# Optimization experiments

Hardware: AMD Instinct MI355X
Metric: run time of the kernel (lower is better)

Reference implementation:

```python
import jax, jax.numpy as jnp
import numpy as np

B, S, E, H = 4, 2048, 1024, 16
D = E // H  # head dim = 64


def setup_inputs() -> dict:
    key = jax.random.key(0)
    ks = jax.random.split(key, 9)
    sc = 1.0 / np.sqrt(E)
    x = jax.random.normal(ks[0], (B, S, E), dtype=jnp.float32)
    # causal mask: 1 = keep, 0 = masked -> -inf (matches masked_fill(mask==0, -inf))
    mask = jnp.broadcast_to(jnp.tril(jnp.ones((S, S), dtype=jnp.int32)), (B, S, S))
    return {
        "x": x,
        "mask": mask,
        "wq": jax.random.normal(ks[1], (E, E), dtype=jnp.float32) * sc,
        "bq": jax.random.normal(ks[2], (E,), dtype=jnp.float32) * sc,
        "wk": jax.random.normal(ks[3], (E, E), dtype=jnp.float32) * sc,
        "bk": jax.random.normal(ks[4], (E,), dtype=jnp.float32) * sc,
        "wv": jax.random.normal(ks[5], (E, E), dtype=jnp.float32) * sc,
        "bv": jax.random.normal(ks[6], (E,), dtype=jnp.float32) * sc,
        "wo": jax.random.normal(ks[7], (E, E), dtype=jnp.float32) * sc,
        "bo": jax.random.normal(ks[8], (E,), dtype=jnp.float32) * sc,
    }


def reference(x, mask, wq, bq, wk, bk, wv, bv, wo, bo):
    # nn.Linear: y = x @ W^T + b
    def proj(w, b):
        y = jnp.einsum('bse,fe->bsf', x, w) + b
        return y.reshape(B, S, H, D).transpose(0, 2, 1, 3)  # [B,H,S,D]

    q = proj(wq, bq)
    k = proj(wk, bk)
    v = proj(wv, bv)
    denom = jnp.asarray(np.sqrt(D), dtype=x.dtype)
    score = jnp.einsum('bhqd,bhkd->bhqk', q, k) / denom  # [B,H,S,S]
    score = jnp.where(mask[:, None, :, :] == 0, jnp.asarray(-jnp.inf, score.dtype), score)
    attn = jax.nn.softmax(score, axis=-1)
    out = jnp.einsum('bhqk,bhkd->bhqd', attn, v)  # [B,H,S,D]
    out = out.transpose(0, 2, 1, 3).reshape(B, S, E)
    return jnp.einsum('bse,fe->bsf', out, wo) + bo
```

## Files before the change

kernel.cpp:

```cpp
#include <hip/hip_runtime.h>
#include <cstdint>
#include <cstddef>

typedef unsigned short u16;
typedef __bf16 bf16;
typedef bf16 bf16x8 __attribute__((ext_vector_type(8)));
typedef bf16 bf16x4 __attribute__((ext_vector_type(4)));
typedef float f32x4 __attribute__((ext_vector_type(4)));
typedef u16 u16x8 __attribute__((ext_vector_type(8)));
typedef u16 u16x4 __attribute__((ext_vector_type(4)));

#define ASYNC16(g, l) __builtin_amdgcn_global_load_lds( \
    (const __attribute__((address_space(1))) void*)(g), \
    (__attribute__((address_space(3))) void*)(l), 16, 0, 0)

#define FENCE asm volatile("" ::: "memory")
#define BARRIER do { FENCE; __builtin_amdgcn_s_barrier(); FENCE; } while (0)
#define WAITVM(n) asm volatile("s_waitcnt vmcnt(" #n ")" ::: "memory")

__device__ __forceinline__ u16 f2bf(float f) {
  bf16 h = (bf16)f;
  return __builtin_bit_cast(u16, h);
}

__device__ __forceinline__ u16x4 pk4(float a, float b, float c, float d) {
  bf16x4 v = { (bf16)a, (bf16)b, (bf16)c, (bf16)d };
  return __builtin_bit_cast(u16x4, v);
}

__device__ __forceinline__ void store_out(u16* p, float v) { *p = f2bf(v); }
__device__ __forceinline__ void store_out(float* p, float v) { *p = v; }

__device__ __forceinline__ f32x4 mfma16(bf16x8 a, bf16x8 b, f32x4 c) {
  return __builtin_amdgcn_mfma_f32_16x16x32_bf16(a, b, c, 0, 0, 0);
}

__global__ void prep(const float* __restrict__ x,  const float* __restrict__ wq,
                     const float* __restrict__ wk, const float* __restrict__ wv,
                     const float* __restrict__ wo, const float* __restrict__ bq,
                     const float* __restrict__ bk,
                     u16* __restrict__ xb, u16* __restrict__ wqkb,
                     u16* __restrict__ wvb, u16* __restrict__ wob,
                     float* __restrict__ bqk, float scl)
{
  const int bid = blockIdx.x, tid = threadIdx.x;
  if (bid < 8192) {
    int i = bid * 256 + tid;
    float4 v = ((const float4*)x)[i];
    ((u16x4*)xb)[i] = pk4(v.x, v.y, v.z, v.w);
  } else if (bid < 12288) {
    int wsel = (bid - 8192) >> 10;
    int i = ((bid - 8192) & 1023) * 256 + tid;
    const float* src = wsel == 0 ? wq : wsel == 1 ? wk : wsel == 2 ? wv : wo;
    u16* dst = wsel == 0 ? wqkb : wsel == 1 ? wqkb + 1048576 : wsel == 2 ? wvb : wob;
    float s = wsel == 0 ? scl : 1.0f;
    float4 v = ((const float4*)src)[i];
    ((u16x4*)dst)[i] = pk4(v.x * s, v.y * s, v.z * s, v.w * s);
  } else {
    for (int i = tid; i < 1024; i += 256) {
      bqk[i] = bq[i] * scl;
      bqk[1024 + i] = bk[i];
    }
  }
}

template <typename OutT>
__device__ __forceinline__ void gemm256(
    u16* sA, u16* sB,
    const u16* __restrict__ A, const u16* __restrict__ Bm,
    const float* __restrict__ bias_col, const float* __restrict__ bias_row,
    OutT* __restrict__ C, int M, int N, int K, int bm, int bn)
{
  const int tid = threadIdx.x;
  const int w = tid >> 6, lane = tid & 63;
  const int quad = lane >> 4, l15 = lane & 15;
  const int wr = w >> 2, wc = w & 3;

  const int srow = tid >> 3;
  const int sslot = (tid & 7) ^ (srow & 7);
  const u16* gA = A + (size_t)(bm * 256 + srow) * K + sslot * 8;
  const u16* gB = Bm + (size_t)(bn * 256 + srow) * K + sslot * 8;
  u16* dA = sA + tid * 8;
  u16* dB = sB + tid * 8;
  const size_t rK64 = (size_t)64 * K, rK128 = (size_t)128 * K;

  auto stageA = [&](int c, int h, int kt) {
    const u16* s = gA + h * rK128 + kt * 64;
    u16* d = dA + c * 16384 + h * 8192;
    ASYNC16(s, d);
    ASYNC16(s + rK64, d + 4096);
  };
  auto stageB = [&](int c, int h, int kt) {
    const u16* s = gB + h * rK128 + kt * 64;
    u16* d = dB + c * 16384 + h * 8192;
    ASYNC16(s, d);
    ASYNC16(s + rK64, d + 4096);
  };

  f32x4 acc[8][4] = {};
  bf16x8 af[4][2];
  bf16x8 bf0[2][2];
  bf16x8 bf1[2][2];

  const int aRow = (wr * 128 + l15) * 64;
  const int bRow = (wc * 64 + l15) * 64;
  const int sw0 = (quad ^ (l15 & 7)) * 8;

#define LDA8(SRC, MH) do { \
    _Pragma("unroll") \
    for (int i = 0; i < 4; i++) { \
      af[i][0] = *(const bf16x8*)((SRC) + aRow + ((MH)*4 + i) * 1024 + sw0); \
      af[i][1] = *(const bf16x8*)((SRC) + aRow + ((MH)*4 + i) * 1024 + (sw0 ^ 32)); \
    } } while (0)

#define LDB4(DST, SRC, NH) do { \
    _Pragma("unroll") \
    for (int j = 0; j < 2; j++) { \
      DST[j][0] = *(const bf16x8*)((SRC) + bRow + ((NH)*2 + j) * 1024 + sw0); \
      DST[j][1] = *(const bf16x8*)((SRC) + bRow + ((NH)*2 + j) * 1024 + (sw0 ^ 32)); \
    } } while (0)

#define MMQ8(MH, NH, BF) do { \
    __builtin_amdgcn_s_setprio(1); \
    _Pragma("unroll") \
    for (int i = 0; i < 4; i++) { \
      acc[(MH)*4+i][(NH)*2+0] = mfma16(af[i][0], BF[0][0], acc[(MH)*4+i][(NH)*2+0]); \
      acc[(MH)*4+i][(NH)*2+0] = mfma16(af[i][1], BF[0][1], acc[(MH)*4+i][(NH)*2+0]); \
      acc[(MH)*4+i][(NH)*2+1] = mfma16(af[i][0], BF[1][0], acc[(MH)*4+i][(NH)*2+1]); \
      acc[(MH)*4+i][(NH)*2+1] = mfma16(af[i][1], BF[1][1], acc[(MH)*4+i][(NH)*2+1]); \
    } \
    __builtin_amdgcn_s_setprio(0); \
  } while (0)

  const int NT = K >> 6, NI = NT >> 1;

  stageB(0, 0, 0); stageB(0, 1, 0);
  stageA(0, 0, 0); stageA(0, 1, 0);
  stageB(1, 0, 1); stageB(1, 1, 1);
  WAITVM(4);
  BARRIER;

  u16* sA0 = sA;         u16* sA1 = sA + 16384;
  u16* sB0 = sB;         u16* sB1 = sB + 16384;

  for (int t = 0; t < NI; ++t) {
    const int k1 = 2 * t + 1, kn = 2 * t + 2, kn1 = 2 * t + 3;
    const bool more = (t + 1 < NI);

    LDA8(sA0, 0); LDB4(bf0, sB0, 0);
    stageA(1, 0, k1);
    BARRIER;
    MMQ8(0, 0, bf0);
    BARRIER;

    LDB4(bf1, sB0, 1);
    stageA(1, 1, k1);
    BARRIER;
    MMQ8(0, 1, bf1);
    BARRIER;

    LDA8(sA0, 1);
    if (more) stageB(0, 0, kn);
    BARRIER;
    MMQ8(1, 1, bf1);
    BARRIER;

    if (more) { stageB(0, 1, kn); WAITVM(4); }
    else      { WAITVM(0); }
    BARRIER;
    MMQ8(1, 0, bf0);
    BARRIER;

    LDA8(sA1, 0); LDB4(bf0, sB1, 0);
    if (more) stageA(0, 0, kn);
    BARRIER;
    MMQ8(0, 0, bf0);
    BARRIER;

    LDB4(bf1, sB1, 1);
    if (more) stageA(0, 1, kn);
    BARRIER;
    MMQ8(0, 1, bf1);
    BARRIER;

    LDA8(sA1, 1);
    if (more) stageB(1, 0, kn1);
    BARRIER;
    MMQ8(1, 1, bf1);
    BARRIER;

    if (more) { stageB(1, 1, kn1); WAITVM(4); }
    BARRIER;
    MMQ8(1, 0, bf0);
    BARRIER;
  }

#pragma unroll
  for (int nt = 0; nt < 4; nt++) {
    const int cc = bn * 256 + wc * 64 + nt * 16 + l15;
    const float bc = bias_col ? bias_col[cc] : 0.f;
#pragma unroll
    for (int mt = 0; mt < 8; mt++) {
      const int r0 = bm * 256 + wr * 128 + mt * 16 + quad * 4;
      f32x4 v = acc[mt][nt];
#pragma unroll
      for (int ri = 0; ri < 4; ri++) {
        const float bb = bc + (bias_row ? bias_row[r0 + ri] : 0.f);
        store_out(&C[(size_t)(r0 + ri) * N + cc], v[ri] + bb);
      }
    }
  }
#undef LDA8
#undef LDB4
#undef MMQ8
}

template <typename OutT>
__device__ __forceinline__ void gemm128(
    u16* sA, u16* sB,
    const u16* __restrict__ A, const u16* __restrict__ Bm,
    const float* __restrict__ bias_col, const float* __restrict__ bias_row,
    OutT* __restrict__ C, int M, int N, int K, int bm, int bn)
{
  const int tid = threadIdx.x;
  const int w = tid >> 6, lane = tid & 63;
  const int quad = lane >> 4, l15 = lane & 15;
  const int wr = w >> 2, wc = w & 3;

  const int srow = tid >> 3;
  const int sslot = (tid & 7) ^ (srow & 7);
  const u16* gA = A + (size_t)(bm * 128 + srow) * K + sslot * 8;
  const u16* gB = Bm + (size_t)(bn * 256 + srow) * K + sslot * 8;
  u16* dA = sA + tid * 8;
  u16* dB = sB + tid * 8;
  const size_t rK64 = (size_t)64 * K;

  auto stage0 = [&](int c, int kt) {
    const u16* a = gA + kt * 64;
    u16* da = dA + c * 8192;
    ASYNC16(a, da);
    ASYNC16(a + rK64, da + 4096);
    ASYNC16(gB + kt * 64, dB + c * 16384);
  };
  auto stage1 = [&](int c, int kt) {
    const u16* b = gB + kt * 64;
    u16* db = dB + c * 16384;
    ASYNC16(b + rK64,     db + 4096);
    ASYNC16(b + 2 * rK64, db + 8192);
    ASYNC16(b + 3 * rK64, db + 12288);
  };

  f32x4 acc[4][4] = {};
  bf16x8 af[4][2];
  bf16x8 bfr[2][2];

  const int aRow = (wr * 64 + l15) * 64;
  const int bRow = (wc * 64 + l15) * 64;
  const int sw0 = (quad ^ (l15 & 7)) * 8;

#define LDA(SRC) do { \
    _Pragma("unroll") \
    for (int i = 0; i < 4; i++) { \
      af[i][0] = *(const bf16x8*)((SRC) + aRow + i * 1024 + sw0); \
      af[i][1] = *(const bf16x8*)((SRC) + aRow + i * 1024 + (sw0 ^ 32)); \
    } } while (0)

#define LDB(SRC, NH) do { \
    _Pragma("unroll") \
    for (int j = 0; j < 2; j++) { \
      bfr[j][0] = *(const bf16x8*)((SRC) + bRow + ((NH)*2 + j) * 1024 + sw0); \
      bfr[j][1] = *(const bf16x8*)((SRC) + bRow + ((NH)*2 + j) * 1024 + (sw0 ^ 32)); \
    } } while (0)

#define MMQ(NH) do { \
    __builtin_amdgcn_s_setprio(1); \
    _Pragma("unroll") \
    for (int i = 0; i < 4; i++) { \
      acc[i][(NH)*2+0] = mfma16(af[i][0], bfr[0][0], acc[i][(NH)*2+0]); \
      acc[i][(NH)*2+0] = mfma16(af[i][1], bfr[0][1], acc[i][(NH)*2+0]); \
      acc[i][(NH)*2+1] = mfma16(af[i][0], bfr[1][0], acc[i][(NH)*2+1]); \
      acc[i][(NH)*2+1] = mfma16(af[i][1], bfr[1][1], acc[i][(NH)*2+1]); \
    } \
    __builtin_amdgcn_s_setprio(0); \
  } while (0)

  const int NT = K >> 6;

  stage0(0, 0); stage1(0, 0);
  stage0(1, 1); stage1(1, 1);
  WAITVM(6);
  BARRIER;

  for (int t = 0; t < NT; ++t) {
    const int c = t % 3, c2 = (t + 2) % 3;
    const bool more = (t + 2 < NT);
    const u16* SA = sA + c * 8192;
    const u16* SB = sB + c * 16384;

    LDA(SA); LDB(SB, 0);
    if (more) stage0(c2, t + 2);
    BARRIER;
    MMQ(0);
    BARRIER;

    LDB(SB, 1);
    if (more) {
      stage1(c2, t + 2);
      WAITVM(6);
    } else if (t == NT - 2) {
      WAITVM(0);
    }
    BARRIER;
    MMQ(1);
    BARRIER;
  }

#pragma unroll
  for (int nh = 0; nh < 2; nh++) {
#pragma unroll
    for (int j = 0; j < 2; j++) {
      const int cc = bn * 256 + wc * 64 + nh * 32 + j * 16 + l15;
      const float bc = bias_col ? bias_col[cc] : 0.f;
#pragma unroll
      for (int i = 0; i < 4; i++) {
        const int r0 = bm * 128 + wr * 64 + i * 16 + quad * 4;
        f32x4 v = acc[i][nh * 2 + j];
#pragma unroll
        for (int ri = 0; ri < 4; ri++) {
          const float bb = bc + (bias_row ? bias_row[r0 + ri] : 0.f);
          store_out(&C[(size_t)(r0 + ri) * N + cc], v[ri] + bb);
        }
      }
    }
  }
#undef LDA
#undef LDB
#undef MMQ
}

__global__ __launch_bounds__(512, 2) void gemm_qkv(
    const u16* __restrict__ xb, const u16* __restrict__ wqkb,
    const u16* __restrict__ wvb, const float* __restrict__ bqk,
    const float* __restrict__ bv, u16* __restrict__ qk, u16* __restrict__ vt)
{
  __shared__ __align__(16) u16 pool[73728];
  const int id = blockIdx.x;
  if (id < 256) {
    gemm256<u16>(pool, pool + 32768, xb, wqkb, bqk, nullptr, qk,
                 8192, 2048, 1024, id >> 3, id & 7);
  } else {
    const int j = id - 256;
    gemm128<u16>(pool, pool + 24576, wvb, xb, nullptr, bv, vt,
                 1024, 8192, 1024, j & 7, j >> 3);
  }
}

__global__ __launch_bounds__(512, 2) void gemm_out(
    const u16* __restrict__ ctx, const u16* __restrict__ wob,
    const float* __restrict__ bo, float* __restrict__ out)
{
  __shared__ __align__(16) u16 sA[3 * 8192];
  __shared__ __align__(16) u16 sB[3 * 16384];
  const int id = blockIdx.x;
  gemm128<float>(sA, sB, ctx, wob, bo, nullptr, out, 8192, 1024, 1024,
                 id >> 2, id & 3);
}

__global__ __launch_bounds__(512, 2) void fattn(
    const u16* __restrict__ QK, const u16* __restrict__ VT, u16* __restrict__ ctx)
{
  __shared__ u16 Kt[2][128 * 64];
  __shared__ u16 Vt[2][64 * 128];
  __shared__ u16 Pt[8 * 16 * 32];

  const int tid = threadIdx.x;
  const int w = tid >> 6, lane = tid & 63;
  const int quad = lane >> 4, l15 = lane & 15;
  const int p = blockIdx.x, h = blockIdx.y, b = blockIdx.z;
  const int nA = p + 1;
  const int sBs = 15 - p;

  const int kr = tid >> 3, kc = (tid & 7) ^ (kr & 7);
  const int vr = tid >> 4, vc = (tid & 15) ^ (vr & 15);

  const u16* QKb = QK + (size_t)b * 2048 * 2048;
  const u16* Kg = QKb + 1024 + h * 64 + kc * 8;
  const u16* Vg = VT + (size_t)(h * 64) * 8192 + b * 2048 + vc * 8;

  u16* Pw = Pt + w * 512;

  bf16x8 ones;
#pragma unroll
  for (int j = 0; j < 8; j++) ones[j] = (bf16)1.0f;

  bf16x8 qfA[2], qfB[2], qcur[2];
#pragma unroll
  for (int ks = 0; ks < 2; ks++) {
    qfA[ks] = *(const bf16x8*)(QKb + (size_t)(p  * 128 + w * 16 + l15) * 2048 +
                               h * 64 + ks * 32 + quad * 8);
    qfB[ks] = *(const bf16x8*)(QKb + (size_t)(sBs * 128 + w * 16 + l15) * 2048 +
                               h * 64 + ks * 32 + quad * 8);
  }
  qcur[0] = qfA[0]; qcur[1] = qfA[1];

  auto stage = [&](int bi, int t) {
#pragma unroll
    for (int s = 0; s < 2; s++) {
      ASYNC16(Kg + (size_t)(t * 128 + s * 64 + kr) * 2048, Kt[bi] + (s * 512 + w * 64) * 8);
      ASYNC16(Vg + (size_t)(s * 32 + vr) * 8192 + t * 128,  Vt[bi] + (s * 512 + w * 64) * 8);
    }
  };

  f32x4 oacc[4] = {};
  f32x4 lacc = {};

  auto epi = [&](int sIdx) {
    float rl = 1.0f / lacc[0];
    size_t row = (size_t)b * 2048 + sIdx * 128 + w * 16 + l15;
#pragma unroll
    for (int dt = 0; dt < 4; dt++) {
      u16x4 o = pk4(oacc[dt][0] * rl, oacc[dt][1] * rl,
                    oacc[dt][2] * rl, oacc[dt][3] * rl);
      *(u16x4*)(ctx + row * 1024 + h * 64 + dt * 16 + quad * 4) = o;
    }
  };

  int sCur = p, tcur = 0;
  stage(0, 0);

  for (int u = 0; u < 17; ++u) {
    const int cur = u & 1;
    if (u < 16) {
      const int tn = (u + 1 == nA) ? 0 : tcur + 1;
      stage(cur ^ 1, tn);
      WAITVM(4);
    } else {
      WAITVM(0);
    }
    BARRIER;

    const u16* Kc = Kt[cur];
    const u16* Vc = Vt[cur];

    f32x4 st[8] = {};
#pragma unroll
    for (int ks = 0; ks < 2; ks++) {
      bf16x8 kf[8];
#pragma unroll
      for (int nt = 0; nt < 8; nt++) {
        int row = nt * 16 + l15;
        kf[nt] = *(const bf16x8*)(Kc + (row * 8 + ((ks * 4 + quad) ^ (row & 7))) * 8);
      }
#pragma unroll
      for (int nt = 0; nt < 8; nt++)
        st[nt] = mfma16(kf[nt], qcur[ks], st[nt]);
    }

    if (tcur == sCur) {
      const int qg = w * 16 + l15;
#pragma unroll
      for (int nt = 0; nt < 8; nt++)
#pragma unroll
        for (int r = 0; r < 4; r++)
          if (nt * 16 + quad * 4 + r > qg) st[nt][r] = -3e38f;
    }
#pragma unroll
    for (int nt = 0; nt < 8; nt++)
#pragma unroll
      for (int r = 0; r < 4; r++)
        st[nt][r] = exp2f(st[nt][r]);

    const int swz = (l15 >> 1) & 3;
#pragma unroll
    for (int hf = 0; hf < 2; hf++) {
#pragma unroll
      for (int ks = 0; ks < 2; ks++) {
#pragma unroll
        for (int j = 0; j < 2; j++) {
          int nt = hf * 4 + ks * 2 + j;
          u16x4 pkv = pk4(st[nt][0], st[nt][1], st[nt][2], st[nt][3]);
          int c = (j * 2 + (quad >> 1)) ^ swz;
          *(u16x4*)(Pw + (l15 << 5) + (c << 3) + ((quad & 1) << 2)) = pkv;
        }
        const int cq = quad ^ swz;
        bf16x8 pf0 = *(const bf16x8*)(Pw + (l15 << 5) + (cq << 3));
        lacc = mfma16(ones, pf0, lacc);
#pragma unroll
        for (int dt = 0; dt < 4; dt++) {
          int vrow = dt * 16 + l15;
          bf16x8 vf = *(const bf16x8*)(Vc + (vrow * 16 + ((hf * 8 + ks * 4 + quad) ^ (vrow & 15))) * 8);
          oacc[dt] = mfma16(vf, pf0, oacc[dt]);
        }
      }
    }
    BARRIER;

    if (u == nA - 1) {
      epi(p);
#pragma unroll
      for (int dt = 0; dt < 4; dt++) oacc[dt] = f32x4{0.f, 0.f, 0.f, 0.f};
      lacc = f32x4{0.f, 0.f, 0.f, 0.f};
      qcur[0] = qfB[0]; qcur[1] = qfB[1];
      sCur = sBs; tcur = 0;
    } else {
      tcur++;
    }
  }

  epi(sBs);
}

extern "C" void kernel_launch(void* const* d_in, const int* in_sizes, int n_in,
                              void* d_out, int out_size, void* d_ws, size_t ws_size,
                              hipStream_t stream)
{
  const float* x  = (const float*)d_in[0];
  const float* wq = (const float*)d_in[2];
  const float* bq = (const float*)d_in[3];
  const float* wk = (const float*)d_in[4];
  const float* bk = (const float*)d_in[5];
  const float* wv = (const float*)d_in[6];
  const float* bv = (const float*)d_in[7];
  const float* wo = (const float*)d_in[8];
  const float* bo = (const float*)d_in[9];

  const float SCL = 0.125f * 1.44269504088896f;

  char* ws = (char*)d_ws;
  u16*   xb   = (u16*)(ws);
  u16*   ctx  = (u16*)(ws);
  u16*   wqkb = (u16*)(ws + 16777216);
  u16*   wvb  = (u16*)(ws + 20971520);
  u16*   wob  = (u16*)(ws + 23068672);
  float* bqk  = (float*)(ws + 25165824);
  u16*   qk   = (u16*)(ws + 25174016);
  u16*   vt   = (u16*)(ws + 58728448);
  float* out  = (float*)d_out;

  prep<<<12289, 256, 0, stream>>>(x, wq, wk, wv, wo, bq, bk,
                                  xb, wqkb, wvb, wob, bqk, SCL);

  gemm_qkv<<<512, 512, 0, stream>>>(xb, wqkb, wvb, bqk, bv, qk, vt);
  fattn<<<dim3(8, 16, 4), 512, 0, stream>>>(qk, vt, ctx);
  gemm_out<<<256, 512, 0, stream>>>(ctx, wob, bo, out);
}
```

Baseline: 302.4 us.

## Halve attention block threads so each wave computes two query row tiles

The flash-attention kernel now runs with 256 threads (4 waves) instead of 512, and each wave handles 32 query rows (two 16-row MFMA tiles) rather than 16. Each K and V fragment read from LDS is therefore reused across two query tiles, which roughly halves LDS read traffic per FLOP, and the async staging loop issues twice as many loads per thread. The cost is higher register pressure from doubled accumulators and scores, and fewer waves per block to hide latency.

```diff
diff --git a/kernel.cpp b/kernel.cpp
--- a/kernel.cpp
+++ b/kernel.cpp
@@ -366,12 +366,12 @@
                  id >> 2, id & 3);
 }
 
-__global__ __launch_bounds__(512, 2) void fattn(
+__global__ __launch_bounds__(256, 2) void fattn(
     const u16* __restrict__ QK, const u16* __restrict__ VT, u16* __restrict__ ctx)
 {
   __shared__ u16 Kt[2][128 * 64];
   __shared__ u16 Vt[2][64 * 128];
-  __shared__ u16 Pt[8 * 16 * 32];
+  __shared__ u16 Pt[4 * 32 * 32];
 
   const int tid = threadIdx.x;
   const int w = tid >> 6, lane = tid & 63;
@@ -380,48 +380,55 @@
   const int nA = p + 1;
   const int sBs = 15 - p;
 
-  const int kr = tid >> 3, kc = (tid & 7) ^ (kr & 7);
-  const int vr = tid >> 4, vc = (tid & 15) ^ (vr & 15);
-
   const u16* QKb = QK + (size_t)b * 2048 * 2048;
-  const u16* Kg = QKb + 1024 + h * 64 + kc * 8;
-  const u16* Vg = VT + (size_t)(h * 64) * 8192 + b * 2048 + vc * 8;
-
-  u16* Pw = Pt + w * 512;
+  const u16* Kg = QKb + 1024 + h * 64 + ((tid & 7) ^ ((tid >> 3) & 7)) * 8;
+  const u16* Vg = VT + (size_t)(h * 64) * 8192 + b * 2048 +
+                  ((tid & 15) ^ ((tid >> 4) & 15)) * 8;
+
+  u16* Pw = Pt + w * 1024;
 
   bf16x8 ones;
 #pragma unroll
   for (int j = 0; j < 8; j++) ones[j] = (bf16)1.0f;
 
-  bf16x8 qfA[2], qfB[2], qcur[2];
-#pragma unroll
-  for (int ks = 0; ks < 2; ks++) {
-    qfA[ks] = *(const bf16x8*)(QKb + (size_t)(p  * 128 + w * 16 + l15) * 2048 +
-                               h * 64 + ks * 32 + quad * 8);
-    qfB[ks] = *(const bf16x8*)(QKb + (size_t)(sBs * 128 + w * 16 + l15) * 2048 +
-                               h * 64 + ks * 32 + quad * 8);
-  }
-  qcur[0] = qfA[0]; qcur[1] = qfA[1];
+  bf16x8 qfA[2][2], qfB[2][2], qcur[2][2];
+#pragma unroll
+  for (int mt = 0; mt < 2; mt++)
+#pragma unroll
+    for (int ks = 0; ks < 2; ks++) {
+      qfA[mt][ks] = *(const bf16x8*)(QKb +
+          (size_t)(p  * 128 + w * 32 + mt * 16 + l15) * 2048 +
+          h * 64 + ks * 32 + quad * 8);
+      qfB[mt][ks] = *(const bf16x8*)(QKb +
+          (size_t)(sBs * 128 + w * 32 + mt * 16 + l15) * 2048 +
+          h * 64 + ks * 32 + quad * 8);
+      qcur[mt][ks] = qfA[mt][ks];
+    }
 
   auto stage = [&](int bi, int t) {
 #pragma unroll
-    for (int s = 0; s < 2; s++) {
-      ASYNC16(Kg + (size_t)(t * 128 + s * 64 + kr) * 2048, Kt[bi] + (s * 512 + w * 64) * 8);
-      ASYNC16(Vg + (size_t)(s * 32 + vr) * 8192 + t * 128,  Vt[bi] + (s * 512 + w * 64) * 8);
+    for (int s = 0; s < 4; s++) {
+      ASYNC16(Kg + (size_t)(t * 128 + s * 32 + (tid >> 3)) * 2048,
+              Kt[bi] + (s * 256 + w * 64) * 8);
+      ASYNC16(Vg + (size_t)(s * 16 + (tid >> 4)) * 8192 + t * 128,
+              Vt[bi] + (s * 256 + w * 64) * 8);
     }
   };
 
-  f32x4 oacc[4] = {};
-  f32x4 lacc = {};
+  f32x4 oacc[4][2] = {};
+  f32x4 lacc[2] = {};
 
   auto epi = [&](int sIdx) {
-    float rl = 1.0f / lacc[0];
-    size_t row = (size_t)b * 2048 + sIdx * 128 + w * 16 + l15;
-#pragma unroll
-    for (int dt = 0; dt < 4; dt++) {
-      u16x4 o = pk4(oacc[dt][0] * rl, oacc[dt][1] * rl,
-                    oacc[dt][2] * rl, oacc[dt][3] * rl);
-      *(u16x4*)(ctx + row * 1024 + h * 64 + dt * 16 + quad * 4) = o;
+#pragma unroll
+    for (int mt = 0; mt < 2; mt++) {
+      float rl = 1.0f / lacc[mt][0];
+      size_t row = (size_t)b * 2048 + sIdx * 128 + w * 32 + mt * 16 + l15;
+#pragma unroll
+      for (int dt = 0; dt < 4; dt++) {
+        u16x4 o = pk4(oacc[dt][mt][0] * rl, oacc[dt][mt][1] * rl,
+                      oacc[dt][mt][2] * rl, oacc[dt][mt][3] * rl);
+        *(u16x4*)(ctx + row * 1024 + h * 64 + dt * 16 + quad * 4) = o;
+      }
     }
   };
 
@@ -433,7 +440,7 @@
     if (u < 16) {
       const int tn = (u + 1 == nA) ? 0 : tcur + 1;
       stage(cur ^ 1, tn);
-      WAITVM(4);
+      WAITVM(8);
     } else {
       WAITVM(0);
     }
@@ -442,7 +449,7 @@
     const u16* Kc = Kt[cur];
     const u16* Vc = Vt[cur];
 
-    f32x4 st[8] = {};
+    f32x4 st[2][8] = {};
 #pragma unroll
     for (int ks = 0; ks < 2; ks++) {
       bf16x8 kf[8];
@@ -452,44 +459,58 @@
         kf[nt] = *(const bf16x8*)(Kc + (row * 8 + ((ks * 4 + quad) ^ (row & 7))) * 8);
       }
 #pragma unroll
+      for (int nt = 0; nt < 8; nt++) {
+        st[0][nt] = mfma16(kf[nt], qcur[0][ks], st[0][nt]);
+        st[1][nt] = mfma16(kf[nt], qcur[1][ks], st[1][nt]);
+      }
+    }
+
+    if (tcur == sCur) {
+#pragma unroll
+      for (int mt = 0; mt < 2; mt++) {
+        const int qg = w * 32 + mt * 16 + l15;
+#pragma unroll
+        for (int nt = 0; nt < 8; nt++)
+#pragma unroll
+          for (int r = 0; r < 4; r++)
+            if (nt * 16 + quad * 4 + r > qg) st[mt][nt][r] = -3e38f;
+      }
+    }
+#pragma unroll
+    for (int mt = 0; mt < 2; mt++)
+#pragma unroll
       for (int nt = 0; nt < 8; nt++)
-        st[nt] = mfma16(kf[nt], qcur[ks], st[nt]);
-    }
-
-    if (tcur == sCur) {
-      const int qg = w * 16 + l15;
-#pragma unroll
-      for (int nt = 0; nt < 8; nt++)
 #pragma unroll
         for (int r = 0; r < 4; r++)
-          if (nt * 16 + quad * 4 + r > qg) st[nt][r] = -3e38f;
-    }
-#pragma unroll
-    for (int nt = 0; nt < 8; nt++)
-#pragma unroll
-      for (int r = 0; r < 4; r++)
-        st[nt][r] = exp2f(st[nt][r]);
-
-    const int swz = (l15 >> 1) & 3;
+          st[mt][nt][r] = exp2f(st[mt][nt][r]);
+
 #pragma unroll
     for (int hf = 0; hf < 2; hf++) {
 #pragma unroll
       for (int ks = 0; ks < 2; ks++) {
 #pragma unroll
-        for (int j = 0; j < 2; j++) {
-          int nt = hf * 4 + ks * 2 + j;
-          u16x4 pkv = pk4(st[nt][0], st[nt][1], st[nt][2], st[nt][3]);
-          int c = (j * 2 + (quad >> 1)) ^ swz;
-          *(u16x4*)(Pw + (l15 << 5) + (c << 3) + ((quad & 1) << 2)) = pkv;
+        for (int mt = 0; mt < 2; mt++) {
+          const int row = mt * 16 + l15;
+          const int swz = (row >> 1) & 3;
+#pragma unroll
+          for (int j = 0; j < 2; j++) {
+            int nt = hf * 4 + ks * 2 + j;
+            u16x4 pkv = pk4(st[mt][nt][0], st[mt][nt][1], st[mt][nt][2], st[mt][nt][3]);
+            int c = (j * 2 + (quad >> 1)) ^ swz;
+            *(u16x4*)(Pw + (row << 5) + (c << 3) + ((quad & 1) << 2)) = pkv;
+          }
         }
-        const int cq = quad ^ swz;
+        const int cq = quad ^ ((l15 >> 1) & 3);
         bf16x8 pf0 = *(const bf16x8*)(Pw + (l15 << 5) + (cq << 3));
-        lacc = mfma16(ones, pf0, lacc);
+        bf16x8 pf1 = *(const bf16x8*)(Pw + ((16 + l15) << 5) + (cq << 3));
+        lacc[0] = mfma16(ones, pf0, lacc[0]);
+        lacc[1] = mfma16(ones, pf1, lacc[1]);
 #pragma unroll
         for (int dt = 0; dt < 4; dt++) {
           int vrow = dt * 16 + l15;
           bf16x8 vf = *(const bf16x8*)(Vc + (vrow * 16 + ((hf * 8 + ks * 4 + quad) ^ (vrow & 15))) * 8);
-          oacc[dt] = mfma16(vf, pf0, oacc[dt]);
+          oacc[dt][0] = mfma16(vf, pf0, oacc[dt][0]);
+          oacc[dt][1] = mfma16(vf, pf1, oacc[dt][1]);
         }
       }
     }
@@ -498,9 +519,16 @@
     if (u == nA - 1) {
       epi(p);
 #pragma unroll
-      for (int dt = 0; dt < 4; dt++) oacc[dt] = f32x4{0.f, 0.f, 0.f, 0.f};
-      lacc = f32x4{0.f, 0.f, 0.f, 0.f};
-      qcur[0] = qfB[0]; qcur[1] = qfB[1];
+      for (int dt = 0; dt < 4; dt++) {
+        oacc[dt][0] = f32x4{0.f, 0.f, 0.f, 0.f};
+        oacc[dt][1] = f32x4{0.f, 0.f, 0.f, 0.f};
+      }
+      lacc[0] = f32x4{0.f, 0.f, 0.f, 0.f};
+      lacc[1] = f32x4{0.f, 0.f, 0.f, 0.f};
+#pragma unroll
+      for (int mt = 0; mt < 2; mt++)
+#pragma unroll
+        for (int ks = 0; ks < 2; ks++) qcur[mt][ks] = qfB[mt][ks];
       sCur = sBs; tcur = 0;
     } else {
       tcur++;
@@ -541,6 +569,6 @@
                                   xb, wqkb, wvb, wob, bqk, SCL);
 
   gemm_qkv<<<512, 512, 0, stream>>>(xb, wqkb, wvb, bqk, bv, qk, vt);
-  fattn<<<dim3(8, 16, 4), 512, 0, stream>>>(qk, vt, ctx);
+  fattn<<<dim3(8, 16, 4), 256, 0, stream>>>(qk, vt, ctx);
   gemm_out<<<256, 512, 0, stream>>>(ctx, wob, bo, out);
 }
```

New measurement: 313.4 us. 1.04x slower.
